# Kernel optimization log

Hardware: AMD Instinct MI355X
Metric: run time of the kernel (lower is better)

Reference implementation:

```python
import jax, jax.numpy as jnp
import numpy as np

B, S, D, H = 2, 2048, 1024, 16
DK = D // H

def setup_inputs() -> dict:
    key = jax.random.key(0)
    ks = jax.random.split(key, 9)
    s = 1.0 / np.sqrt(D)
    return {
        "query": jax.random.normal(ks[0], (B, S, D), dtype=jnp.float32),
        "Wq": jax.random.uniform(ks[1], (D, D), jnp.float32, -s, s),
        "bq": jax.random.uniform(ks[2], (D,), jnp.float32, -s, s),
        "Wk": jax.random.uniform(ks[3], (D, D), jnp.float32, -s, s),
        "bk": jax.random.uniform(ks[4], (D,), jnp.float32, -s, s),
        "Wv": jax.random.uniform(ks[5], (D, D), jnp.float32, -s, s),
        "bv": jax.random.uniform(ks[6], (D,), jnp.float32, -s, s),
        "Wo": jax.random.uniform(ks[7], (D, D), jnp.float32, -s, s),
        "bo": jax.random.uniform(ks[8], (D,), jnp.float32, -s, s),
    }

def reference(query, Wq, bq, Wk, bk, Wv, bv, Wo, bo):
    # q/k/v projections, reshape to [B,H,S,DK]
    def proj(x, W, b):
        return (x @ W + b).reshape(B, S, H, DK).transpose(0, 2, 1, 3)
    q = proj(query, Wq, bq)
    k = proj(query, Wk, bk)
    v = proj(query, Wv, bv)
    scores = jnp.einsum("bhqd,bhkd->bhqk", q, k) / jnp.sqrt(jnp.float32(DK))
    attn = jax.nn.softmax(scores, axis=-1)
    out = jnp.einsum("bhqk,bhkd->bhqd", attn, v)  # [B,H,S,DK]
    concat = out.transpose(0, 2, 1, 3).reshape(B, S, D)
    return concat @ Wo + bo
```

## Files before the change

kernel.cpp:

```cpp
#include <hip/hip_runtime.h>

#define S_LEN  2048
#define DMODEL 1024
#define NHEAD  16
#define DKDIM  64
#define NBATCH 2

typedef short bf16x8 __attribute__((ext_vector_type(8)));
typedef float f32x4  __attribute__((ext_vector_type(4)));

__device__ __forceinline__ unsigned short f2b(float f){
  unsigned int x = __float_as_uint(f);
  return (unsigned short)((x + 0x7FFFu + ((x >> 16) & 1u)) >> 16);
}
__device__ __forceinline__ unsigned short f2b_rhu(float f){
  return (unsigned short)((__float_as_uint(f) + 0x8000u) >> 16);
}
__device__ __forceinline__ bf16x8 ld8(const unsigned short* p){
  return *reinterpret_cast<const bf16x8*>(p);
}
__device__ __forceinline__ void gld16(const unsigned short* g, unsigned short* l){
  __builtin_amdgcn_global_load_lds(
      (const __attribute__((address_space(1))) unsigned int*)(uintptr_t)g,
      (__attribute__((address_space(3))) unsigned int*)(uintptr_t)l,
      16, 0, 0);
}

__global__ __launch_bounds__(256) void convert_x(
    const float* __restrict__ X, unsigned short* __restrict__ Xc)
{
  const size_t i0 = ((size_t)blockIdx.x * 256 + threadIdx.x) * 8;
  const float4 a = *reinterpret_cast<const float4*>(X + i0);
  const float4 b = *reinterpret_cast<const float4*>(X + i0 + 4);
  bf16x8 o;
  o[0]=(short)f2b(a.x); o[1]=(short)f2b(a.y); o[2]=(short)f2b(a.z); o[3]=(short)f2b(a.w);
  o[4]=(short)f2b(b.x); o[5]=(short)f2b(b.y); o[6]=(short)f2b(b.z); o[7]=(short)f2b(b.w);
  *reinterpret_cast<bf16x8*>(Xc + i0) = o;
}

__global__ __launch_bounds__(256) void transpose_w(
    const float* __restrict__ W0, const float* __restrict__ W1,
    const float* __restrict__ W2, const float* __restrict__ W3,
    unsigned short* __restrict__ Wt)
{
  __shared__ unsigned short tile[64][65];
  const float* src = (blockIdx.z==0)?W0:(blockIdx.z==1)?W1:(blockIdx.z==2)?W2:W3;
  unsigned short* dst = Wt + (size_t)blockIdx.z * DMODEL * DMODEL;
  const int r0 = blockIdx.x * 64, c0 = blockIdx.y * 64;
  #pragma unroll
  for(int t=0;t<16;t++){
    int idx = threadIdx.x + t*256;
    int r = idx >> 6, c = idx & 63;
    tile[r][c] = f2b(src[(size_t)(r0+r)*DMODEL + (c0+c)]);
  }
  __syncthreads();
  #pragma unroll
  for(int t=0;t<16;t++){
    int idx = threadIdx.x + t*256;
    int r = idx >> 6, c = idx & 63;
    dst[(size_t)(c0+r)*DMODEL + (r0+c)] = tile[c][r];
  }
}

__global__ __launch_bounds__(256) void gemm_qkv(
    const unsigned short* __restrict__ Xc,
    const unsigned short* __restrict__ WtBase,
    const float* __restrict__ bq,
    const float* __restrict__ bk,
    const float* __restrict__ bv,
    unsigned short* __restrict__ q_ws,
    unsigned short* __restrict__ k_ws,
    unsigned short* __restrict__ vT_ws)
{
  __shared__ __align__(16) unsigned short sA[128][32];
  __shared__ __align__(16) unsigned short sB[128][32];
  const int z = blockIdx.z;
  const unsigned short* Wt   = WtBase + (size_t)z * DMODEL * DMODEL;
  const float* bias = (z==0) ? bq : ((z==1) ? bk : bv);
  const int m0 = blockIdx.x * 128, n0 = blockIdx.y * 128;
  const int tid = threadIdx.x;
  const int w = tid >> 6, lane = tid & 63, quad = lane >> 4, lm = lane & 15;
  const int wm = (w & 1) * 64, wn = (w >> 1) * 64;
  const int srow = lane >> 2, scol = (lane & 3) * 8;

  f32x4 acc[4][4];
  #pragma unroll
  for(int i=0;i<4;i++)
    #pragma unroll
    for(int j=0;j<4;j++){ f32x4 z4 = {0.f,0.f,0.f,0.f}; acc[i][j] = z4; }

  for(int k0=0;k0<DMODEL;k0+=32){
    #pragma unroll
    for(int j=0;j<2;j++){
      gld16(Xc + (size_t)(m0 + w*32 + j*16 + srow)*DMODEL + k0 + scol, &sA[w*32 + j*16][0]);
      gld16(Wt + (size_t)(n0 + w*32 + j*16 + srow)*DMODEL + k0 + scol, &sB[w*32 + j*16][0]);
    }
    __syncthreads();
    bf16x8 a[4], b[4];
    #pragma unroll
    for(int i=0;i<4;i++) a[i] = ld8(&sA[wm + i*16 + lm][quad*8]);
    #pragma unroll
    for(int j=0;j<4;j++) b[j] = ld8(&sB[wn + j*16 + lm][quad*8]);
    #pragma unroll
    for(int i=0;i<4;i++)
      #pragma unroll
      for(int j=0;j<4;j++)
        acc[i][j] = __builtin_amdgcn_mfma_f32_16x16x32_bf16(a[i], b[j], acc[i][j], 0, 0, 0);
    __syncthreads();
  }

  #pragma unroll
  for(int j=0;j<4;j++){
    const int n  = n0 + wn + j*16 + lm;
    const float bb = bias[n];
    const int h_ = n >> 6, d_ = n & 63;
    #pragma unroll
    for(int i=0;i<4;i++){
      #pragma unroll
      for(int r=0;r<4;r++){
        const int m  = m0 + wm + i*16 + quad*4 + r;
        const int b_ = m >> 11, s_ = m & 2047;
        const unsigned short o = f2b(acc[i][j][r] + bb);
        if(z == 0)      q_ws [((size_t)(b_*NHEAD + h_)*S_LEN + s_)*DKDIM + d_] = o;
        else if(z == 1) k_ws [((size_t)(b_*NHEAD + h_)*S_LEN + s_)*DKDIM + d_] = o;
        else            vT_ws[((size_t)(b_*NHEAD + h_)*DKDIM + d_)*S_LEN + s_] = o;
      }
    }
  }
}

__global__ __launch_bounds__(256) void flash_attn(
    const unsigned short* __restrict__ q_ws,
    const unsigned short* __restrict__ k_ws,
    const unsigned short* __restrict__ vT_ws,
    unsigned short* __restrict__ attn_c)
{
  __shared__ __align__(16) unsigned short kt[2][64][72];
  __shared__ __align__(16) unsigned short vt[2][64][72];
  __shared__ __align__(16) unsigned short p_lds[4][32][72];
  const int bh = blockIdx.y;
  const int b_ = bh >> 4, h_ = bh & 15;
  const int tid = threadIdx.x;
  const int w = tid >> 6, lane = tid & 63, quad = lane >> 4, lm = lane & 15;
  const int r0 = blockIdx.x * 128 + w * 32;

  const unsigned short* qp = q_ws  + ((size_t)bh * S_LEN + r0) * DKDIM;
  const unsigned short* kp = k_ws  + (size_t)bh * S_LEN * DKDIM;
  const unsigned short* vp = vT_ws + (size_t)bh * DKDIM * S_LEN;

  bf16x8 qf[2][2];
  #pragma unroll
  for(int g=0;g<2;g++)
    #pragma unroll
    for(int c=0;c<2;c++)
      qf[g][c] = ld8(qp + (size_t)(g*16 + lm)*DKDIM + c*32 + quad*8);

  f32x4 o_acc[2][4];
  #pragma unroll
  for(int g=0;g<2;g++)
    #pragma unroll
    for(int d=0;d<4;d++){ f32x4 z4 = {0.f,0.f,0.f,0.f}; o_acc[g][d] = z4; }
  float rsum[2][4] = {{0.f,0.f,0.f,0.f},{0.f,0.f,0.f,0.f}};

  const int srow = lane >> 3;
  const int scol = (lane & 7) * 8;

  bf16x8 kreg[2], vreg[2];
  #pragma unroll
  for(int p=0;p<2;p++){
    kreg[p] = ld8(kp + (size_t)(w*16 + p*8 + srow)*DKDIM + scol);
    vreg[p] = ld8(vp + (size_t)(w*16 + p*8 + srow)*S_LEN + scol);
  }
  #pragma unroll
  for(int p=0;p<2;p++){
    *reinterpret_cast<bf16x8*>(&kt[0][w*16 + p*8 + srow][scol]) = kreg[p];
    *reinterpret_cast<bf16x8*>(&vt[0][w*16 + p*8 + srow][scol]) = vreg[p];
  }
  __syncthreads();

  for(int t=0;t<32;t++){
    const int buf = t & 1;
    if(t < 31){
      const int jn = (t+1)*64;
      #pragma unroll
      for(int p=0;p<2;p++){
        kreg[p] = ld8(kp + (size_t)(jn + w*16 + p*8 + srow)*DKDIM + scol);
        vreg[p] = ld8(vp + (size_t)(w*16 + p*8 + srow)*S_LEN + jn + scol);
      }
    }
    #pragma unroll
    for(int s=0;s<4;s++){
      bf16x8 k0 = ld8(&kt[buf][s*16 + lm][quad*8]);
      bf16x8 k1 = ld8(&kt[buf][s*16 + lm][32 + quad*8]);
      #pragma unroll
      for(int g=0;g<2;g++){
        f32x4 z4 = {0.f,0.f,0.f,0.f};
        f32x4 sc = __builtin_amdgcn_mfma_f32_16x16x32_bf16(qf[g][0], k0, z4, 0,0,0);
        sc       = __builtin_amdgcn_mfma_f32_16x16x32_bf16(qf[g][1], k1, sc, 0,0,0);
        #pragma unroll
        for(int r=0;r<4;r++){
          float e = __expf(sc[r]*0.125f);
          rsum[g][r] += e;
          p_lds[w][g*16 + quad*4 + r][s*16 + lm] = f2b_rhu(e);
        }
      }
    }
    #pragma unroll
    for(int ch=0;ch<2;ch++){
      bf16x8 pf0 = ld8(&p_lds[w][lm     ][ch*32 + quad*8]);
      bf16x8 pf1 = ld8(&p_lds[w][16 + lm][ch*32 + quad*8]);
      #pragma unroll
      for(int d=0;d<4;d++){
        bf16x8 vf = ld8(&vt[buf][d*16 + lm][ch*32 + quad*8]);
        o_acc[0][d] = __builtin_amdgcn_mfma_f32_16x16x32_bf16(pf0, vf, o_acc[0][d], 0,0,0);
        o_acc[1][d] = __builtin_amdgcn_mfma_f32_16x16x32_bf16(pf1, vf, o_acc[1][d], 0,0,0);
      }
    }
    if(t < 31){
      const int nb = 1 - buf;
      #pragma unroll
      for(int p=0;p<2;p++){
        *reinterpret_cast<bf16x8*>(&kt[nb][w*16 + p*8 + srow][scol]) = kreg[p];
        *reinterpret_cast<bf16x8*>(&vt[nb][w*16 + p*8 + srow][scol]) = vreg[p];
      }
    }
    __syncthreads();
  }

  float rinv[2][4];
  #pragma unroll
  for(int g=0;g<2;g++)
    #pragma unroll
    for(int r=0;r<4;r++){
      float s = rsum[g][r];
      s += __shfl_xor(s,1);
      s += __shfl_xor(s,2);
      s += __shfl_xor(s,4);
      s += __shfl_xor(s,8);
      rinv[g][r] = __frcp_rn(s);
    }

  #pragma unroll
  for(int g=0;g<2;g++)
    #pragma unroll
    for(int d=0;d<4;d++)
      #pragma unroll
      for(int r=0;r<4;r++){
        const int row = r0 + g*16 + quad*4 + r;
        const int col = h_*DKDIM + d*16 + lm;
        attn_c[((size_t)(b_*S_LEN + row))*DMODEL + col] = f2b(o_acc[g][d][r] * rinv[g][r]);
      }
}

__global__ __launch_bounds__(256) void gemm_out(
    const unsigned short* __restrict__ A,
    const unsigned short* __restrict__ Wt,
    const float* __restrict__ bias,
    float* __restrict__ out)
{
  __shared__ __align__(16) unsigned short sA[128][32];
  __shared__ __align__(16) unsigned short sB[128][32];
  const int m0 = blockIdx.x * 128, n0 = blockIdx.y * 128;
  const int tid = threadIdx.x;
  const int w = tid >> 6, lane = tid & 63, quad = lane >> 4, lm = lane & 15;
  const int wm = (w & 1) * 64, wn = (w >> 1) * 64;
  const int srow = lane >> 2, scol = (lane & 3) * 8;

  f32x4 acc[4][4];
  #pragma unroll
  for(int i=0;i<4;i++)
    #pragma unroll
    for(int j=0;j<4;j++){ f32x4 z4 = {0.f,0.f,0.f,0.f}; acc[i][j] = z4; }

  for(int k0=0;k0<DMODEL;k0+=32){
    #pragma unroll
    for(int j=0;j<2;j++){
      gld16(A  + (size_t)(m0 + w*32 + j*16 + srow)*DMODEL + k0 + scol, &sA[w*32 + j*16][0]);
      gld16(Wt + (size_t)(n0 + w*32 + j*16 + srow)*DMODEL + k0 + scol, &sB[w*32 + j*16][0]);
    }
    __syncthreads();
    bf16x8 a[4], b[4];
    #pragma unroll
    for(int i=0;i<4;i++) a[i] = ld8(&sA[wm + i*16 + lm][quad*8]);
    #pragma unroll
    for(int j=0;j<4;j++) b[j] = ld8(&sB[wn + j*16 + lm][quad*8]);
    #pragma unroll
    for(int i=0;i<4;i++)
      #pragma unroll
      for(int j=0;j<4;j++)
        acc[i][j] = __builtin_amdgcn_mfma_f32_16x16x32_bf16(a[i], b[j], acc[i][j], 0, 0, 0);
    __syncthreads();
  }

  #pragma unroll
  for(int j=0;j<4;j++){
    const int n = n0 + wn + j*16 + lm;
    const float bb = bias[n];
    #pragma unroll
    for(int i=0;i<4;i++){
      #pragma unroll
      for(int r=0;r<4;r++){
        const int m = m0 + wm + i*16 + quad*4 + r;
        out[(size_t)m*DMODEL + n] = acc[i][j][r] + bb;
      }
    }
  }
}

extern "C" void kernel_launch(void* const* d_in, const int* in_sizes, int n_in,
                              void* d_out, int out_size, void* d_ws, size_t ws_size,
                              hipStream_t stream)
{
  const float* X  = (const float*)d_in[0];
  const float* Wq = (const float*)d_in[1];
  const float* bq = (const float*)d_in[2];
  const float* Wk = (const float*)d_in[3];
  const float* bk = (const float*)d_in[4];
  const float* Wv = (const float*)d_in[5];
  const float* bv = (const float*)d_in[6];
  const float* Wo = (const float*)d_in[7];
  const float* bo = (const float*)d_in[8];

  unsigned short* ws = (unsigned short*)d_ws;
  const size_t WMAT = (size_t)DMODEL * DMODEL;
  const size_t QKV  = (size_t)NBATCH * NHEAD * S_LEN * DKDIM;
  unsigned short* Wt     = ws;
  unsigned short* Xc     = ws + 4*WMAT;
  unsigned short* q_ws   = Xc + QKV;
  unsigned short* k_ws   = q_ws + QKV;
  unsigned short* vT_ws  = k_ws + QKV;
  unsigned short* attn_c = Xc;
  float* out = (float*)d_out;

  convert_x  <<<dim3(2048),     256, 0, stream>>>(X, Xc);
  transpose_w<<<dim3(16,16,4),  256, 0, stream>>>(Wq, Wk, Wv, Wo, Wt);
  gemm_qkv   <<<dim3(32,8,3),   256, 0, stream>>>(Xc, Wt, bq, bk, bv, q_ws, k_ws, vT_ws);
  flash_attn <<<dim3(16,32),    256, 0, stream>>>(q_ws, k_ws, vT_ws, attn_c);
  gemm_out   <<<dim3(32,8),     256, 0, stream>>>(attn_c, Wt + 3*WMAT, bo, out);
}
```

Measured before the change: 216.1 us.

## Merge prep kernels, fold softmax scale into Wq, shrink output GEMM tile

Merges the X conversion and weight transpose into a single launch. Folds the 1/sqrt(dk)*log2(e) factor into Wq and bq, so the attention inner loop can use exp2f on raw scores without a multiply. Halves the M tile of the output projection GEMM to 64 rows, doubling the grid to 512 blocks for better CU occupancy. The pre-scaled Q is rounded to bf16, which slightly changes rounding compared with scaling after the matmul.

Measured after the change: 224.9 us. 4.0% more time.

```diff
diff --git a/kernel.cpp b/kernel.cpp
--- a/kernel.cpp
+++ b/kernel.cpp
@@ -5,6 +5,7 @@
 #define NHEAD  16
 #define DKDIM  64
 #define NBATCH 2
+#define SCALE_Q 0.1803368801f
 
 typedef short bf16x8 __attribute__((ext_vector_type(8)));
 typedef float f32x4  __attribute__((ext_vector_type(4)));
@@ -26,32 +27,35 @@
       16, 0, 0);
 }
 
-__global__ __launch_bounds__(256) void convert_x(
-    const float* __restrict__ X, unsigned short* __restrict__ Xc)
-{
-  const size_t i0 = ((size_t)blockIdx.x * 256 + threadIdx.x) * 8;
-  const float4 a = *reinterpret_cast<const float4*>(X + i0);
-  const float4 b = *reinterpret_cast<const float4*>(X + i0 + 4);
-  bf16x8 o;
-  o[0]=(short)f2b(a.x); o[1]=(short)f2b(a.y); o[2]=(short)f2b(a.z); o[3]=(short)f2b(a.w);
-  o[4]=(short)f2b(b.x); o[5]=(short)f2b(b.y); o[6]=(short)f2b(b.z); o[7]=(short)f2b(b.w);
-  *reinterpret_cast<bf16x8*>(Xc + i0) = o;
-}
-
-__global__ __launch_bounds__(256) void transpose_w(
+__global__ __launch_bounds__(256) void prep(
+    const float* __restrict__ X, unsigned short* __restrict__ Xc,
     const float* __restrict__ W0, const float* __restrict__ W1,
     const float* __restrict__ W2, const float* __restrict__ W3,
     unsigned short* __restrict__ Wt)
 {
   __shared__ unsigned short tile[64][65];
-  const float* src = (blockIdx.z==0)?W0:(blockIdx.z==1)?W1:(blockIdx.z==2)?W2:W3;
-  unsigned short* dst = Wt + (size_t)blockIdx.z * DMODEL * DMODEL;
-  const int r0 = blockIdx.x * 64, c0 = blockIdx.y * 64;
+  const int bid = blockIdx.x;
+  if(bid < 2048){
+    const size_t i0 = ((size_t)bid * 256 + threadIdx.x) * 8;
+    const float4 a = *reinterpret_cast<const float4*>(X + i0);
+    const float4 b = *reinterpret_cast<const float4*>(X + i0 + 4);
+    bf16x8 o;
+    o[0]=(short)f2b(a.x); o[1]=(short)f2b(a.y); o[2]=(short)f2b(a.z); o[3]=(short)f2b(a.w);
+    o[4]=(short)f2b(b.x); o[5]=(short)f2b(b.y); o[6]=(short)f2b(b.z); o[7]=(short)f2b(b.w);
+    *reinterpret_cast<bf16x8*>(Xc + i0) = o;
+    return;
+  }
+  const int t2 = bid - 2048;
+  const int z  = t2 >> 8, rem = t2 & 255, bx = rem & 15, by = rem >> 4;
+  const float* src = (z==0)?W0:(z==1)?W1:(z==2)?W2:W3;
+  const float sc = (z==0) ? SCALE_Q : 1.0f;
+  unsigned short* dst = Wt + (size_t)z * DMODEL * DMODEL;
+  const int r0 = bx * 64, c0 = by * 64;
   #pragma unroll
   for(int t=0;t<16;t++){
     int idx = threadIdx.x + t*256;
     int r = idx >> 6, c = idx & 63;
-    tile[r][c] = f2b(src[(size_t)(r0+r)*DMODEL + (c0+c)]);
+    tile[r][c] = f2b(src[(size_t)(r0+r)*DMODEL + (c0+c)] * sc);
   }
   __syncthreads();
   #pragma unroll
@@ -77,6 +81,7 @@
   const int z = blockIdx.z;
   const unsigned short* Wt   = WtBase + (size_t)z * DMODEL * DMODEL;
   const float* bias = (z==0) ? bq : ((z==1) ? bk : bv);
+  const float bscale = (z==0) ? SCALE_Q : 1.0f;
   const int m0 = blockIdx.x * 128, n0 = blockIdx.y * 128;
   const int tid = threadIdx.x;
   const int w = tid >> 6, lane = tid & 63, quad = lane >> 4, lm = lane & 15;
@@ -112,7 +117,7 @@
   #pragma unroll
   for(int j=0;j<4;j++){
     const int n  = n0 + wn + j*16 + lm;
-    const float bb = bias[n];
+    const float bb = bias[n] * bscale;
     const int h_ = n >> 6, d_ = n & 63;
     #pragma unroll
     for(int i=0;i<4;i++){
@@ -199,7 +204,7 @@
         sc       = __builtin_amdgcn_mfma_f32_16x16x32_bf16(qf[g][1], k1, sc, 0,0,0);
         #pragma unroll
         for(int r=0;r<4;r++){
-          float e = __expf(sc[r]*0.125f);
+          float e = exp2f(sc[r]);
           rsum[g][r] += e;
           p_lds[w][g*16 + quad*4 + r][s*16 + lm] = f2b_rhu(e);
         }
@@ -258,34 +263,33 @@
     const float* __restrict__ bias,
     float* __restrict__ out)
 {
-  __shared__ __align__(16) unsigned short sA[128][32];
+  __shared__ __align__(16) unsigned short sA[64][32];
   __shared__ __align__(16) unsigned short sB[128][32];
-  const int m0 = blockIdx.x * 128, n0 = blockIdx.y * 128;
+  const int m0 = blockIdx.x * 64, n0 = blockIdx.y * 128;
   const int tid = threadIdx.x;
   const int w = tid >> 6, lane = tid & 63, quad = lane >> 4, lm = lane & 15;
-  const int wm = (w & 1) * 64, wn = (w >> 1) * 64;
+  const int wm = (w & 1) * 32, wn = (w >> 1) * 64;
   const int srow = lane >> 2, scol = (lane & 3) * 8;
 
-  f32x4 acc[4][4];
-  #pragma unroll
-  for(int i=0;i<4;i++)
+  f32x4 acc[2][4];
+  #pragma unroll
+  for(int i=0;i<2;i++)
     #pragma unroll
     for(int j=0;j<4;j++){ f32x4 z4 = {0.f,0.f,0.f,0.f}; acc[i][j] = z4; }
 
   for(int k0=0;k0<DMODEL;k0+=32){
-    #pragma unroll
-    for(int j=0;j<2;j++){
-      gld16(A  + (size_t)(m0 + w*32 + j*16 + srow)*DMODEL + k0 + scol, &sA[w*32 + j*16][0]);
+    gld16(A + (size_t)(m0 + w*16 + srow)*DMODEL + k0 + scol, &sA[w*16][0]);
+    #pragma unroll
+    for(int j=0;j<2;j++)
       gld16(Wt + (size_t)(n0 + w*32 + j*16 + srow)*DMODEL + k0 + scol, &sB[w*32 + j*16][0]);
-    }
-    __syncthreads();
-    bf16x8 a[4], b[4];
-    #pragma unroll
-    for(int i=0;i<4;i++) a[i] = ld8(&sA[wm + i*16 + lm][quad*8]);
+    __syncthreads();
+    bf16x8 a[2], b[4];
+    #pragma unroll
+    for(int i=0;i<2;i++) a[i] = ld8(&sA[wm + i*16 + lm][quad*8]);
     #pragma unroll
     for(int j=0;j<4;j++) b[j] = ld8(&sB[wn + j*16 + lm][quad*8]);
     #pragma unroll
-    for(int i=0;i<4;i++)
+    for(int i=0;i<2;i++)
       #pragma unroll
       for(int j=0;j<4;j++)
         acc[i][j] = __builtin_amdgcn_mfma_f32_16x16x32_bf16(a[i], b[j], acc[i][j], 0, 0, 0);
@@ -297,7 +301,7 @@
     const int n = n0 + wn + j*16 + lm;
     const float bb = bias[n];
     #pragma unroll
-    for(int i=0;i<4;i++){
+    for(int i=0;i<2;i++){
       #pragma unroll
       for(int r=0;r<4;r++){
         const int m = m0 + wm + i*16 + quad*4 + r;
@@ -332,9 +336,8 @@
   unsigned short* attn_c = Xc;
   float* out = (float*)d_out;
 
-  convert_x  <<<dim3(2048),     256, 0, stream>>>(X, Xc);
-  transpose_w<<<dim3(16,16,4),  256, 0, stream>>>(Wq, Wk, Wv, Wo, Wt);
-  gemm_qkv   <<<dim3(32,8,3),   256, 0, stream>>>(Xc, Wt, bq, bk, bv, q_ws, k_ws, vT_ws);
-  flash_attn <<<dim3(16,32),    256, 0, stream>>>(q_ws, k_ws, vT_ws, attn_c);
-  gemm_out   <<<dim3(32,8),     256, 0, stream>>>(attn_c, Wt + 3*WMAT, bo, out);
-}
+  prep      <<<dim3(3072),     256, 0, stream>>>(X, Xc, Wq, Wk, Wv, Wo, Wt);
+  gemm_qkv  <<<dim3(32,8,3),   256, 0, stream>>>(Xc, Wt, bq, bk, bv, q_ws, k_ws, vT_ws);
+  flash_attn<<<dim3(16,32),    256, 0, stream>>>(q_ws, k_ws, vT_ws, attn_c);
+  gemm_out  <<<dim3(64,8),     256, 0, stream>>>(attn_c, Wt + 3*WMAT, bo, out);
+}
```
